# Optimization experiments

Measured on AMD Instinct MI355X. Metric: run time of the kernel, lower is better.

## Reference

```python
import jax, jax.numpy as jnp
import numpy as np

N = 50000
E = 800000
IN_CH = 128
HID = 64
HEADS = 4
G = 64  # number of graphs in batch
NEG_SLOPE = 0.2


def setup_inputs() -> dict:
    key = jax.random.key(0)
    ks = jax.random.split(key, 16)
    s = lambda fan_in: 1.0 / np.sqrt(fan_in)
    x = jax.random.normal(ks[0], (N, IN_CH), dtype=jnp.float32)
    edge_index = jax.random.randint(ks[1], (2, E), 0, N, dtype=jnp.int64)
    batch = jnp.sort(jax.random.randint(ks[2], (N,), 0, G, dtype=jnp.int64))
    # GAT layer 1: in 128 -> heads*hid = 256
    W1 = jax.random.uniform(ks[3], (IN_CH, HEADS * HID), jnp.float32, -s(IN_CH), s(IN_CH))
    a1_src = jax.random.uniform(ks[4], (HEADS, HID), jnp.float32, -s(HID), s(HID))
    a1_dst = jax.random.uniform(ks[5], (HEADS, HID), jnp.float32, -s(HID), s(HID))
    b1 = jnp.zeros((HEADS * HID,), jnp.float32)
    # GAT layer 2: in 256 -> heads*hid = 256
    W2 = jax.random.uniform(ks[6], (HEADS * HID, HEADS * HID), jnp.float32, -s(HEADS * HID), s(HEADS * HID))
    a2_src = jax.random.uniform(ks[7], (HEADS, HID), jnp.float32, -s(HID), s(HID))
    a2_dst = jax.random.uniform(ks[8], (HEADS, HID), jnp.float32, -s(HID), s(HID))
    b2 = jnp.zeros((HEADS * HID,), jnp.float32)
    # post-pool MLP: (in + 2*heads*hid) -> 256 -> 128
    d_cat = IN_CH + 2 * HEADS * HID
    W3 = jax.random.uniform(ks[9], (d_cat, 256), jnp.float32, -s(d_cat), s(d_cat))
    b3 = jnp.zeros((256,), jnp.float32)
    W4 = jax.random.uniform(ks[10], (256, 128), jnp.float32, -s(256), s(256))
    b4 = jnp.zeros((128,), jnp.float32)
    return {"x": x, "edge_index": edge_index, "batch": batch,
            "W1": W1, "a1_src": a1_src, "a1_dst": a1_dst, "b1": b1,
            "W2": W2, "a2_src": a2_src, "a2_dst": a2_dst, "b2": b2,
            "W3": W3, "b3": b3, "W4": W4, "b4": b4}


def gat_layer(x, src, dst, W, a_src, a_dst, b):
    n = x.shape[0]
    h = (x @ W).reshape(n, HEADS, HID)                 # [N,H,D]
    e_src = jnp.einsum('nhd,hd->nh', h, a_src)         # [N,H]
    e_dst = jnp.einsum('nhd,hd->nh', h, a_dst)
    e = jax.nn.leaky_relu(e_src[src] + e_dst[dst], NEG_SLOPE)  # [E,H]
    # segment softmax over incoming edges of each destination node
    m = jax.ops.segment_max(e, dst, num_segments=n)
    m = jnp.where(jnp.isfinite(m), m, 0.0)
    ex = jnp.exp(e - m[dst])
    denom = jax.ops.segment_sum(ex, dst, num_segments=n)
    alpha = ex / (denom[dst] + 1e-16)                  # [E,H]
    msg = h[src] * alpha[:, :, None]                   # [E,H,D]
    out = jax.ops.segment_sum(msg, dst, num_segments=n)
    return out.reshape(n, HEADS * HID) + b


def reference(x, edge_index, batch, W1, a1_src, a1_dst, b1, W2, a2_src, a2_dst, b2, W3, b3, W4, b4):
    src, dst = edge_index[0], edge_index[1]
    h0 = x
    h1 = jax.nn.relu(gat_layer(h0, src, dst, W1, a1_src, a1_dst, b1))
    h2 = jax.nn.relu(gat_layer(h1, src, dst, W2, a2_src, a2_dst, b2))
    comb = jnp.concatenate([h0, h1, h2], axis=-1)      # [N, 128+256+256]
    sums = jax.ops.segment_sum(comb, batch, num_segments=G)
    cnt = jax.ops.segment_sum(jnp.ones((x.shape[0],), comb.dtype), batch, num_segments=G)
    pooled = sums / jnp.maximum(cnt, 1.0)[:, None]     # [G, 640]
    hmlp = jax.nn.relu(pooled @ W3 + b3)               # dropout is identity at eval
    return hmlp @ W4 + b4                              # [G, 128]
```

## Files before the change

### kernel.cpp

```cpp
#include <hip/hip_runtime.h>
#include <cstdint>
#include <cstddef>

#define N_NODES 50000
#define M_PAD 50048
#define E_EDGES 800000
#define INCH 128
#define HID 64
#define HEADS 4
#define NHD 256
#define NGRAPH 64
#define DCAT 640
#define NEG_SLOPE 0.2f

typedef __attribute__((ext_vector_type(8))) short bf16x8;
typedef __attribute__((ext_vector_type(4))) float f32x4;

static __device__ inline unsigned short f2bf(float f) {
    unsigned int u = __float_as_uint(f);
    unsigned int r = (u + 0x7FFFu + ((u >> 16) & 1u)) >> 16;
    return (unsigned short)r;
}
static __device__ inline float bf2f(unsigned short b) {
    return __uint_as_float(((unsigned int)b) << 16);
}

#define W1N (INCH * NHD)
#define W2N (NHD * NHD)
#define XN  (N_NODES * INCH)
#define HB  ((E_EDGES + 255) / 256)
#define GB  ((N_NODES + 255) / 256)
#define PZB ((NGRAPH * DCAT + 255) / 256)
#define SPB ((W1N + W2N + XN + 255) / 256)
#define PREPB (HB + GB + PZB + SPB)

__global__ void prep_kernel(
    const int* __restrict__ ei, const int* __restrict__ batch,
    const float* __restrict__ W1, const float* __restrict__ W2,
    const float* __restrict__ x,
    int* __restrict__ counts, int* __restrict__ goff,
    float* __restrict__ psums,
    unsigned short* __restrict__ w1thi, unsigned short* __restrict__ w1tlo,
    unsigned short* __restrict__ w2thi, unsigned short* __restrict__ w2tlo,
    unsigned short* __restrict__ xhi, unsigned short* __restrict__ xlo)
{
    const int b = blockIdx.x;
    if (b < HB) {
        const int e = b * 256 + threadIdx.x;
        if (e < E_EDGES) atomicAdd(&counts[ei[E_EDGES + e]], 1);
        return;
    }
    if (b < HB + GB) {
        const int n = (b - HB) * 256 + threadIdx.x;
        if (n >= N_NODES) return;
        const int bb = batch[n];
        const int bp = (n == 0) ? -1 : batch[n - 1];
        for (int g = bp + 1; g <= bb; ++g) goff[g] = n;
        if (n == N_NODES - 1)
            for (int g = bb + 1; g <= NGRAPH; ++g) goff[g] = N_NODES;
        return;
    }
    if (b < HB + GB + PZB) {
        const int i = (b - HB - GB) * 256 + threadIdx.x;
        if (i < NGRAPH * DCAT) psums[i] = 0.f;
        return;
    }
    const int i = (b - HB - GB - PZB) * 256 + threadIdx.x;
    float v; unsigned short* dhi; unsigned short* dlo; int idx;
    if (i < W1N) {
        const int n = i / INCH, k = i - n * INCH;
        v = W1[(size_t)k * NHD + n]; dhi = w1thi; dlo = w1tlo; idx = i;
    } else if (i < W1N + W2N) {
        const int j = i - W1N;
        const int n = j / NHD, k = j - n * NHD;
        v = W2[(size_t)k * NHD + n]; dhi = w2thi; dlo = w2tlo; idx = j;
    } else {
        const int j = i - W1N - W2N;
        if (j >= XN) return;
        v = x[j]; dhi = xhi; dlo = xlo; idx = j;
    }
    const unsigned short h = f2bf(v);
    dhi[idx] = h;
    dlo[idx] = f2bf(v - bf2f(h));
}

#define GK 64
#define LDAB 72

__global__ __launch_bounds__(256, 2) void gemm_mfma(
    const unsigned short* __restrict__ Athi,
    const unsigned short* __restrict__ Atlo,
    const unsigned short* __restrict__ Bthi,
    const unsigned short* __restrict__ Btlo,
    const float* __restrict__ asrc, const float* __restrict__ adst,
    unsigned short* __restrict__ Cb, float* __restrict__ es,
    float* __restrict__ ed, int M, int K)
{
    __shared__ unsigned short Ahi[128 * LDAB];
    __shared__ unsigned short Alo[128 * LDAB];
    __shared__ unsigned short Bhi[128 * LDAB];
    __shared__ unsigned short Blo[128 * LDAB];

    const int t    = threadIdx.x;
    const int row0 = blockIdx.x * 128;
    const int col0 = blockIdx.y * 128;
    const int wave = t >> 6, lane = t & 63;
    const int wr = (wave >> 1) * 64;
    const int wc = (wave & 1) * 64;
    const int m16 = lane & 15, quad = lane >> 4;

    f32x4 acc[4][4];
#pragma unroll
    for (int i = 0; i < 4; ++i)
#pragma unroll
        for (int j = 0; j < 4; ++j) acc[i][j] = (f32x4){0.f, 0.f, 0.f, 0.f};

    for (int k0 = 0; k0 < K; k0 += GK) {
#pragma unroll
        for (int i = 0; i < 4; ++i) {
            const int seg = t + i * 256;
            const int r = seg >> 3, p = (seg & 7) * 8;
            const size_t ga = (size_t)(row0 + r) * K + k0 + p;
            const size_t gb = (size_t)(col0 + r) * K + k0 + p;
            *(int4*)(&Ahi[r * LDAB + p]) = *(const int4*)(Athi + ga);
            *(int4*)(&Alo[r * LDAB + p]) = *(const int4*)(Atlo + ga);
            *(int4*)(&Bhi[r * LDAB + p]) = *(const int4*)(Bthi + gb);
            *(int4*)(&Blo[r * LDAB + p]) = *(const int4*)(Btlo + gb);
        }
        __syncthreads();

#pragma unroll
        for (int h = 0; h < 2; ++h) {
            bf16x8 afh[4], afl[4], bfh[4], bfl[4];
#pragma unroll
            for (int i = 0; i < 4; ++i) {
                const int r = wr + i * 16 + m16;
                afh[i] = *(const bf16x8*)(&Ahi[r * LDAB + h * 32 + quad * 8]);
                afl[i] = *(const bf16x8*)(&Alo[r * LDAB + h * 32 + quad * 8]);
            }
#pragma unroll
            for (int j = 0; j < 4; ++j) {
                const int n = wc + j * 16 + m16;
                bfh[j] = *(const bf16x8*)(&Bhi[n * LDAB + h * 32 + quad * 8]);
                bfl[j] = *(const bf16x8*)(&Blo[n * LDAB + h * 32 + quad * 8]);
            }
#pragma unroll
            for (int i = 0; i < 4; ++i)
#pragma unroll
                for (int j = 0; j < 4; ++j) {
                    acc[i][j] = __builtin_amdgcn_mfma_f32_16x16x32_bf16(afh[i], bfh[j], acc[i][j], 0, 0, 0);
                    acc[i][j] = __builtin_amdgcn_mfma_f32_16x16x32_bf16(afh[i], bfl[j], acc[i][j], 0, 0, 0);
                    acc[i][j] = __builtin_amdgcn_mfma_f32_16x16x32_bf16(afl[i], bfh[j], acc[i][j], 0, 0, 0);
                }
        }
        __syncthreads();
    }

#pragma unroll
    for (int i = 0; i < 4; ++i)
#pragma unroll
        for (int reg = 0; reg < 4; ++reg) {
            const int r = row0 + wr + i * 16 + quad * 4 + reg;
            if (r < M) {
#pragma unroll
                for (int j = 0; j < 4; ++j)
                    Cb[(size_t)r * NHD + col0 + wc + j * 16 + m16] = f2bf(acc[i][j][reg]);
            }
        }

    const int head = (col0 + wc) >> 6;
    float a_s[4], a_d[4];
#pragma unroll
    for (int j = 0; j < 4; ++j) {
        a_s[j] = asrc[head * HID + j * 16 + m16];
        a_d[j] = adst[head * HID + j * 16 + m16];
    }
#pragma unroll
    for (int i = 0; i < 4; ++i)
#pragma unroll
        for (int reg = 0; reg < 4; ++reg) {
            float ps = 0.f, pd = 0.f;
#pragma unroll
            for (int j = 0; j < 4; ++j) {
                const float v = acc[i][j][reg];
                ps += v * a_s[j];
                pd += v * a_d[j];
            }
#pragma unroll
            for (int off = 1; off < 16; off <<= 1) {
                ps += __shfl_xor(ps, off, 64);
                pd += __shfl_xor(pd, off, 64);
            }
            if (m16 == 0) {
                const int r = row0 + wr + i * 16 + quad * 4 + reg;
                if (r < M) {
                    es[r * HEADS + head] = ps;
                    ed[r * HEADS + head] = pd;
                }
            }
        }
}

#define SBLK 1024
#define NSCB ((N_NODES + SBLK - 1) / SBLK)

__global__ __launch_bounds__(1024) void scan_local_kernel(
    const int* __restrict__ counts, int* __restrict__ offsets,
    int* __restrict__ bsum)
{
    __shared__ int tmp[SBLK];
    const int t = threadIdx.x;
    const int i = blockIdx.x * SBLK + t;
    const int v = (i < N_NODES) ? counts[i] : 0;
    tmp[t] = v;
    __syncthreads();
    for (int off = 1; off < SBLK; off <<= 1) {
        const int u = (t >= off) ? tmp[t - off] : 0;
        __syncthreads();
        tmp[t] += u;
        __syncthreads();
    }
    if (i < N_NODES) offsets[i] = tmp[t] - v;
    if (t == SBLK - 1) bsum[blockIdx.x] = tmp[t];
}

__global__ __launch_bounds__(1024) void scan_final_kernel(
    int* __restrict__ offsets, int* __restrict__ cursor,
    const int* __restrict__ bsum)
{
    __shared__ int base_sh;
    const int b = blockIdx.x;
    if (threadIdx.x == 0) {
        int s = 0;
        for (int j = 0; j < b; ++j) s += bsum[j];
        base_sh = s;
    }
    __syncthreads();
    const int i = b * SBLK + threadIdx.x;
    if (i < N_NODES) {
        const int v = offsets[i] + base_sh;
        offsets[i] = v;
        cursor[i]  = v;
    }
    if (b == 0 && threadIdx.x == 0) offsets[N_NODES] = E_EDGES;
}

__global__ void scatter_kernel(const int* __restrict__ ei, int* __restrict__ cursor,
                               int* __restrict__ csr)
{
    const int e = blockIdx.x * 256 + threadIdx.x;
    if (e >= E_EDGES) return;
    const int s = ei[e];
    const int d = ei[E_EDGES + e];
    const int pos = atomicAdd(&cursor[d], 1);
    csr[pos] = s;
}

__global__ __launch_bounds__(256) void aggregate_fused(
    const unsigned short* __restrict__ hb, const int* __restrict__ csr,
    const int* __restrict__ offsets,
    const float* __restrict__ es, const float* __restrict__ ed,
    const float* __restrict__ bias, unsigned short* __restrict__ outhi,
    unsigned short* __restrict__ outlo)
{
    const int wid  = threadIdx.x >> 6;
    const int lane = threadIdx.x & 63;
    const int node = blockIdx.x * 4 + wid;
    if (node >= N_NODES) return;
    const int head = lane >> 4;
    const int col  = lane * 4;
    const int sub  = lane & 15;

    const float edc = ed[node * 4 + head];
    const int beg = offsets[node], end = offsets[node + 1];

    float4 acc = make_float4(0.f, 0.f, 0.f, 0.f);
    float dsum = 0.f;

    int base = beg;
    int m_cur = min(16, end - base);
    int s_cur = 0; float w_cur = 0.f;
    if (base < end && sub < m_cur) {
        s_cur = csr[base + sub];
        float u = es[s_cur * 4 + head] + edc;
        u = u > 0.f ? u : NEG_SLOPE * u;
        w_cur = expf(u);
    }

    while (base < end) {
        const int base_n = base + 16;
        const int m_nxt = min(16, end - base_n);
        int s_nxt = 0; float w_nxt = 0.f;
        if (base_n < end && sub < m_nxt) {
            s_nxt = csr[base_n + sub];
            float u = es[s_nxt * 4 + head] + edc;
            u = u > 0.f ? u : NEG_SLOPE * u;
            w_nxt = expf(u);
        }
        if (m_cur == 16) {
#pragma unroll
            for (int i = 0; i < 16; ++i) {
                const int   s = (int)__builtin_amdgcn_readlane((unsigned)s_cur, i);
                const float w = __shfl(w_cur, (lane & 48) + i, 64);
                const ushort4 v = *(const ushort4*)(hb + (size_t)s * NHD + col);
                acc.x += w * bf2f(v.x);
                acc.y += w * bf2f(v.y);
                acc.z += w * bf2f(v.z);
                acc.w += w * bf2f(v.w);
                dsum += w;
            }
        } else {
            for (int i = 0; i < m_cur; ++i) {
                const int   s = __shfl(s_cur, i, 64);
                const float w = __shfl(w_cur, (lane & 48) + i, 64);
                const ushort4 v = *(const ushort4*)(hb + (size_t)s * NHD + col);
                acc.x += w * bf2f(v.x);
                acc.y += w * bf2f(v.y);
                acc.z += w * bf2f(v.z);
                acc.w += w * bf2f(v.w);
                dsum += w;
            }
        }
        s_cur = s_nxt; w_cur = w_nxt; m_cur = m_nxt; base = base_n;
    }

    const float inv = 1.0f / (dsum + 1e-16f);
    const float4 bb = *(const float4*)(bias + col);
    float4 o;
    o.x = fmaxf(acc.x * inv + bb.x, 0.f);
    o.y = fmaxf(acc.y * inv + bb.y, 0.f);
    o.z = fmaxf(acc.z * inv + bb.z, 0.f);
    o.w = fmaxf(acc.w * inv + bb.w, 0.f);
    ushort4 oh;
    oh.x = f2bf(o.x); oh.y = f2bf(o.y); oh.z = f2bf(o.z); oh.w = f2bf(o.w);
    *(ushort4*)(outhi + (size_t)node * NHD + col) = oh;
    if (outlo) {
        ushort4 ol;
        ol.x = f2bf(o.x - bf2f(oh.x));
        ol.y = f2bf(o.y - bf2f(oh.y));
        ol.z = f2bf(o.z - bf2f(oh.z));
        ol.w = f2bf(o.w - bf2f(oh.w));
        *(ushort4*)(outlo + (size_t)node * NHD + col) = ol;
    }
}

#define PRB 128

__global__ __launch_bounds__(640) void pool_sum_kernel(
    const unsigned short* __restrict__ xhi, const unsigned short* __restrict__ h1b,
    const unsigned short* __restrict__ h2b, const int* __restrict__ batch,
    float* __restrict__ sums)
{
    __shared__ int bsh[PRB];
    const int c  = threadIdx.x;
    const int r0 = blockIdx.x * PRB;
    const int r1 = min(N_NODES, r0 + PRB);
    const int nr = r1 - r0;
    if (c < nr) bsh[c] = batch[r0 + c];
    __syncthreads();

    const unsigned short* srcb; int ld, cc;
    if (c < INCH)            { srcb = xhi; ld = INCH; cc = c; }
    else if (c < INCH + NHD) { srcb = h1b; ld = NHD;  cc = c - INCH; }
    else                     { srcb = h2b; ld = NHD;  cc = c - INCH - NHD; }

    float sum = 0.f;
    int g = bsh[0];
    for (int i = 0; i < nr; ++i) {
        const int gb = bsh[i];
        if (gb != g) {
            atomicAdd(&sums[g * DCAT + c], sum);
            sum = 0.f;
            g = gb;
        }
        sum += bf2f(srcb[(size_t)(r0 + i) * ld + cc]);
    }
    atomicAdd(&sums[g * DCAT + c], sum);
}

__global__ __launch_bounds__(256) void mlp_kernel(
    const float* __restrict__ psums, const int* __restrict__ goff,
    const float* __restrict__ W3, const float* __restrict__ b3,
    const float* __restrict__ W4, const float* __restrict__ b4,
    float* __restrict__ out)
{
    const int g0 = blockIdx.x * 8;
    __shared__ float p[8][DCAT];
    __shared__ float hm[8][256];
    for (int idx = threadIdx.x; idx < 8 * DCAT; idx += 256) {
        const int gg = idx / DCAT, i = idx - gg * DCAT;
        const int g = g0 + gg;
        const float inv = 1.0f / fmaxf((float)(goff[g + 1] - goff[g]), 1.0f);
        p[gg][i] = psums[(size_t)g * DCAT + i] * inv;
    }
    __syncthreads();
    const int c = threadIdx.x;
    float acc[8];
#pragma unroll
    for (int gg = 0; gg < 8; ++gg) acc[gg] = b3[c];
    for (int k = 0; k < DCAT; ++k) {
        const float w = W3[(size_t)k * 256 + c];
#pragma unroll
        for (int gg = 0; gg < 8; ++gg) acc[gg] += p[gg][k] * w;
    }
#pragma unroll
    for (int gg = 0; gg < 8; ++gg) hm[gg][c] = fmaxf(acc[gg], 0.f);
    __syncthreads();
    const int c2 = threadIdx.x & 127;
    const int gh = (threadIdx.x >> 7) * 4;
    float a2[4];
#pragma unroll
    for (int j = 0; j < 4; ++j) a2[j] = b4[c2];
    for (int k = 0; k < 256; ++k) {
        const float w = W4[(size_t)k * 128 + c2];
#pragma unroll
        for (int j = 0; j < 4; ++j) a2[j] += hm[gh + j][k] * w;
    }
#pragma unroll
    for (int j = 0; j < 4; ++j)
        out[(size_t)(g0 + gh + j) * 128 + c2] = a2[j];
}

extern "C" void kernel_launch(void* const* d_in, const int* in_sizes, int n_in,
                              void* d_out, int out_size, void* d_ws, size_t ws_size,
                              hipStream_t stream)
{
    const float* x     = (const float*)d_in[0];
    const int*   ei    = (const int*)d_in[1];
    const int*   batch = (const int*)d_in[2];
    const float* W1    = (const float*)d_in[3];
    const float* a1s   = (const float*)d_in[4];
    const float* a1d   = (const float*)d_in[5];
    const float* b1    = (const float*)d_in[6];
    const float* W2    = (const float*)d_in[7];
    const float* a2s   = (const float*)d_in[8];
    const float* a2d   = (const float*)d_in[9];
    const float* b2    = (const float*)d_in[10];
    const float* W3    = (const float*)d_in[11];
    const float* b3    = (const float*)d_in[12];
    const float* W4    = (const float*)d_in[13];
    const float* b4    = (const float*)d_in[14];
    float* out = (float*)d_out;

    size_t off = 0;
    auto carve = [&](size_t bytes) -> void* {
        void* p = (char*)d_ws + off;
        off = (off + bytes + 255) & ~(size_t)255;
        return p;
    };
    unsigned short* xhi   = (unsigned short*)carve((size_t)M_PAD * INCH * 2);
    unsigned short* xlo   = (unsigned short*)carve((size_t)M_PAD * INCH * 2);
    unsigned short* ghi   = (unsigned short*)carve((size_t)N_NODES * NHD * 2);
    unsigned short* h1hi  = (unsigned short*)carve((size_t)M_PAD * NHD * 2);
    unsigned short* h1lo  = (unsigned short*)carve((size_t)M_PAD * NHD * 2);
    unsigned short* h2hi  = (unsigned short*)carve((size_t)N_NODES * NHD * 2);
    float* es     = (float*)carve((size_t)N_NODES * HEADS * 4);
    float* ed     = (float*)carve((size_t)N_NODES * HEADS * 4);
    float* psums  = (float*)carve((size_t)NGRAPH * DCAT * 4);
    int*   counts  = (int*)carve((size_t)N_NODES * 4);
    int*   offsets = (int*)carve((size_t)(N_NODES + 1) * 4);
    int*   cursor  = (int*)carve((size_t)N_NODES * 4);
    int*   csr     = (int*)carve((size_t)E_EDGES * 4);
    int*   goff    = (int*)carve((size_t)(NGRAPH + 1) * 4);
    int*   bsum    = (int*)carve((size_t)NSCB * 4);
    unsigned short* w1thi = (unsigned short*)carve((size_t)NHD * INCH * 2);
    unsigned short* w1tlo = (unsigned short*)carve((size_t)NHD * INCH * 2);
    unsigned short* w2thi = (unsigned short*)carve((size_t)NHD * NHD * 2);
    unsigned short* w2tlo = (unsigned short*)carve((size_t)NHD * NHD * 2);

    const int egrid = (E_EDGES + 255) / 256;

    hipMemsetAsync(counts, 0, (size_t)N_NODES * 4, stream);
    prep_kernel<<<PREPB, 256, 0, stream>>>(ei, batch, W1, W2, x,
                                           counts, goff, psums,
                                           w1thi, w1tlo, w2thi, w2tlo, xhi, xlo);
    scan_local_kernel<<<NSCB, SBLK, 0, stream>>>(counts, offsets, bsum);
    scan_final_kernel<<<NSCB, SBLK, 0, stream>>>(offsets, cursor, bsum);
    scatter_kernel<<<egrid, 256, 0, stream>>>(ei, cursor, csr);

    dim3 ggrid((M_PAD + 127) / 128, NHD / 128);

    gemm_mfma<<<ggrid, 256, 0, stream>>>(xhi, xlo, w1thi, w1tlo, a1s, a1d,
                                         ghi, es, ed, N_NODES, INCH);
    aggregate_fused<<<(N_NODES + 3) / 4, 256, 0, stream>>>(ghi, csr, offsets,
                                                           es, ed, b1, h1hi, h1lo);
    gemm_mfma<<<ggrid, 256, 0, stream>>>(h1hi, h1lo, w2thi, w2tlo, a2s, a2d,
                                         ghi, es, ed, N_NODES, NHD);
    aggregate_fused<<<(N_NODES + 3) / 4, 256, 0, stream>>>(ghi, csr, offsets,
                                                           es, ed, b2, h2hi, nullptr);

    pool_sum_kernel<<<(N_NODES + PRB - 1) / PRB, 640, 0, stream>>>(xhi, h1hi, h2hi, batch, psums);
    mlp_kernel<<<NGRAPH / 8, 256, 0, stream>>>(psums, goff, W3, b3, W4, b4, out);
}
```

Measured before the change: 486.6 us.

## Widen GEMM tile to full 256 output columns, halve K step

The GEMM block now covers all 256 output columns (128x256 tile) with a 1D grid, so each A tile is loaded from global memory once instead of twice. The K step is cut from 64 to 32 to keep shared memory in check, and each wave holds 4x8 accumulators. The epilogue computes attention logits for two heads per wave. This costs more registers per thread and more K-loop iterations and barriers, which may lower occupancy under the launch bound of 2 blocks.

```diff
diff --git a/kernel.cpp b/kernel.cpp
--- a/kernel.cpp
+++ b/kernel.cpp
@@ -84,8 +84,8 @@
     dlo[idx] = f2bf(v - bf2f(h));
 }
 
-#define GK 64
-#define LDAB 72
+#define GK 32
+#define LDA 40
 
 __global__ __launch_bounds__(256, 2) void gemm_mfma(
     const unsigned short* __restrict__ Athi,
@@ -96,62 +96,61 @@
     unsigned short* __restrict__ Cb, float* __restrict__ es,
     float* __restrict__ ed, int M, int K)
 {
-    __shared__ unsigned short Ahi[128 * LDAB];
-    __shared__ unsigned short Alo[128 * LDAB];
-    __shared__ unsigned short Bhi[128 * LDAB];
-    __shared__ unsigned short Blo[128 * LDAB];
+    __shared__ unsigned short Ahi[128 * LDA];
+    __shared__ unsigned short Alo[128 * LDA];
+    __shared__ unsigned short Bhi[256 * LDA];
+    __shared__ unsigned short Blo[256 * LDA];
 
     const int t    = threadIdx.x;
     const int row0 = blockIdx.x * 128;
-    const int col0 = blockIdx.y * 128;
     const int wave = t >> 6, lane = t & 63;
-    const int wr = (wave >> 1) * 64;
-    const int wc = (wave & 1) * 64;
+    const int wr  = (wave >> 1) * 64;
+    const int wc2 = (wave & 1) * 128;
     const int m16 = lane & 15, quad = lane >> 4;
 
-    f32x4 acc[4][4];
+    f32x4 acc[4][8];
 #pragma unroll
     for (int i = 0; i < 4; ++i)
 #pragma unroll
-        for (int j = 0; j < 4; ++j) acc[i][j] = (f32x4){0.f, 0.f, 0.f, 0.f};
+        for (int j = 0; j < 8; ++j) acc[i][j] = (f32x4){0.f, 0.f, 0.f, 0.f};
 
     for (int k0 = 0; k0 < K; k0 += GK) {
+#pragma unroll
+        for (int i = 0; i < 2; ++i) {
+            const int seg = t + i * 256;
+            const int r = seg >> 2, p = (seg & 3) * 8;
+            const size_t ga = (size_t)(row0 + r) * K + k0 + p;
+            *(int4*)(&Ahi[r * LDA + p]) = *(const int4*)(Athi + ga);
+            *(int4*)(&Alo[r * LDA + p]) = *(const int4*)(Atlo + ga);
+        }
 #pragma unroll
         for (int i = 0; i < 4; ++i) {
             const int seg = t + i * 256;
-            const int r = seg >> 3, p = (seg & 7) * 8;
-            const size_t ga = (size_t)(row0 + r) * K + k0 + p;
-            const size_t gb = (size_t)(col0 + r) * K + k0 + p;
-            *(int4*)(&Ahi[r * LDAB + p]) = *(const int4*)(Athi + ga);
-            *(int4*)(&Alo[r * LDAB + p]) = *(const int4*)(Atlo + ga);
-            *(int4*)(&Bhi[r * LDAB + p]) = *(const int4*)(Bthi + gb);
-            *(int4*)(&Blo[r * LDAB + p]) = *(const int4*)(Btlo + gb);
+            const int r = seg >> 2, p = (seg & 3) * 8;
+            const size_t gb = (size_t)r * K + k0 + p;
+            *(int4*)(&Bhi[r * LDA + p]) = *(const int4*)(Bthi + gb);
+            *(int4*)(&Blo[r * LDA + p]) = *(const int4*)(Btlo + gb);
         }
         __syncthreads();
 
-#pragma unroll
-        for (int h = 0; h < 2; ++h) {
-            bf16x8 afh[4], afl[4], bfh[4], bfl[4];
+        bf16x8 afh[4], afl[4];
+#pragma unroll
+        for (int i = 0; i < 4; ++i) {
+            const int r = wr + i * 16 + m16;
+            afh[i] = *(const bf16x8*)(&Ahi[r * LDA + quad * 8]);
+            afl[i] = *(const bf16x8*)(&Alo[r * LDA + quad * 8]);
+        }
+#pragma unroll
+        for (int j = 0; j < 8; ++j) {
+            const int n = wc2 + j * 16 + m16;
+            const bf16x8 bh = *(const bf16x8*)(&Bhi[n * LDA + quad * 8]);
+            const bf16x8 bl = *(const bf16x8*)(&Blo[n * LDA + quad * 8]);
 #pragma unroll
             for (int i = 0; i < 4; ++i) {
-                const int r = wr + i * 16 + m16;
-                afh[i] = *(const bf16x8*)(&Ahi[r * LDAB + h * 32 + quad * 8]);
-                afl[i] = *(const bf16x8*)(&Alo[r * LDAB + h * 32 + quad * 8]);
-            }
-#pragma unroll
-            for (int j = 0; j < 4; ++j) {
-                const int n = wc + j * 16 + m16;
-                bfh[j] = *(const bf16x8*)(&Bhi[n * LDAB + h * 32 + quad * 8]);
-                bfl[j] = *(const bf16x8*)(&Blo[n * LDAB + h * 32 + quad * 8]);
-            }
-#pragma unroll
-            for (int i = 0; i < 4; ++i)
-#pragma unroll
-                for (int j = 0; j < 4; ++j) {
-                    acc[i][j] = __builtin_amdgcn_mfma_f32_16x16x32_bf16(afh[i], bfh[j], acc[i][j], 0, 0, 0);
-                    acc[i][j] = __builtin_amdgcn_mfma_f32_16x16x32_bf16(afh[i], bfl[j], acc[i][j], 0, 0, 0);
-                    acc[i][j] = __builtin_amdgcn_mfma_f32_16x16x32_bf16(afl[i], bfh[j], acc[i][j], 0, 0, 0);
-                }
+                acc[i][j] = __builtin_amdgcn_mfma_f32_16x16x32_bf16(afh[i], bh, acc[i][j], 0, 0, 0);
+                acc[i][j] = __builtin_amdgcn_mfma_f32_16x16x32_bf16(afh[i], bl, acc[i][j], 0, 0, 0);
+                acc[i][j] = __builtin_amdgcn_mfma_f32_16x16x32_bf16(afl[i], bh, acc[i][j], 0, 0, 0);
+            }
         }
         __syncthreads();
     }
@@ -163,39 +162,48 @@
             const int r = row0 + wr + i * 16 + quad * 4 + reg;
             if (r < M) {
 #pragma unroll
-                for (int j = 0; j < 4; ++j)
-                    Cb[(size_t)r * NHD + col0 + wc + j * 16 + m16] = f2bf(acc[i][j][reg]);
-            }
-        }
-
-    const int head = (col0 + wc) >> 6;
-    float a_s[4], a_d[4];
+                for (int j = 0; j < 8; ++j)
+                    Cb[(size_t)r * NHD + wc2 + j * 16 + m16] = f2bf(acc[i][j][reg]);
+            }
+        }
+
+    const int hbase = wc2 >> 6;
+    float a_s0[4], a_d0[4], a_s1[4], a_d1[4];
 #pragma unroll
     for (int j = 0; j < 4; ++j) {
-        a_s[j] = asrc[head * HID + j * 16 + m16];
-        a_d[j] = adst[head * HID + j * 16 + m16];
+        a_s0[j] = asrc[hbase * HID + j * 16 + m16];
+        a_d0[j] = adst[hbase * HID + j * 16 + m16];
+        a_s1[j] = asrc[(hbase + 1) * HID + j * 16 + m16];
+        a_d1[j] = adst[(hbase + 1) * HID + j * 16 + m16];
     }
 #pragma unroll
     for (int i = 0; i < 4; ++i)
 #pragma unroll
         for (int reg = 0; reg < 4; ++reg) {
-            float ps = 0.f, pd = 0.f;
+            float ps0 = 0.f, pd0 = 0.f, ps1 = 0.f, pd1 = 0.f;
 #pragma unroll
             for (int j = 0; j < 4; ++j) {
-                const float v = acc[i][j][reg];
-                ps += v * a_s[j];
-                pd += v * a_d[j];
+                const float v0 = acc[i][j][reg];
+                const float v1 = acc[i][j + 4][reg];
+                ps0 += v0 * a_s0[j];
+                pd0 += v0 * a_d0[j];
+                ps1 += v1 * a_s1[j];
+                pd1 += v1 * a_d1[j];
             }
 #pragma unroll
             for (int off = 1; off < 16; off <<= 1) {
-                ps += __shfl_xor(ps, off, 64);
-                pd += __shfl_xor(pd, off, 64);
+                ps0 += __shfl_xor(ps0, off, 64);
+                pd0 += __shfl_xor(pd0, off, 64);
+                ps1 += __shfl_xor(ps1, off, 64);
+                pd1 += __shfl_xor(pd1, off, 64);
             }
             if (m16 == 0) {
                 const int r = row0 + wr + i * 16 + quad * 4 + reg;
                 if (r < M) {
-                    es[r * HEADS + head] = ps;
-                    ed[r * HEADS + head] = pd;
+                    es[r * HEADS + hbase]     = ps0;
+                    ed[r * HEADS + hbase]     = pd0;
+                    es[r * HEADS + hbase + 1] = ps1;
+                    ed[r * HEADS + hbase + 1] = pd1;
                 }
             }
         }
@@ -478,7 +486,7 @@
     scan_final_kernel<<<NSCB, SBLK, 0, stream>>>(offsets, cursor, bsum);
     scatter_kernel<<<egrid, 256, 0, stream>>>(ei, cursor, csr);
 
-    dim3 ggrid((M_PAD + 127) / 128, NHD / 128);
+    const int ggrid = M_PAD / 128;
 
     gemm_mfma<<<ggrid, 256, 0, stream>>>(xhi, xlo, w1thi, w1tlo, a1s, a1d,
                                          ghi, es, ed, N_NODES, INCH);
```

Result: no change. 486.4 us (-0.0%).
